# Kernel optimization log

Measured on AMD Instinct MI355X. Metric: run time of the kernel, lower is better.

Reference implementation:

```python
import jax, jax.numpy as jnp
import numpy as np

EPS = 1e-12  # F.normalize eps

def _l2norm(t):
    n = jnp.linalg.norm(t, axis=-1, keepdims=True)
    return t / jnp.maximum(n, EPS)

def setup_inputs() -> dict:
    key = jax.random.key(0)
    ks = jax.random.split(key, 6)
    B, S, H, M = 4, 4096, 1024, 256
    x = jax.random.normal(ks[0], (B, S, H), dtype=jnp.float32)
    W_query = jax.random.normal(ks[1], (M, H), dtype=jnp.float32) * 0.02
    W_key = jax.random.normal(ks[2], (M, H), dtype=jnp.float32) * 0.02
    W_value = jax.random.normal(ks[3], (M, H), dtype=jnp.float32) * 0.02
    W_out = jax.random.normal(ks[4], (H, M), dtype=jnp.float32) * 0.02
    M0 = jnp.zeros((M, M), dtype=jnp.float32)
    return {"x": x, "W_query": W_query, "W_key": W_key, "W_value": W_value,
            "W_out": W_out, "M0": M0, "chunk_size": 64}

def reference(x, W_query, W_key, W_value, W_out, M0, chunk_size):
    B, S, H = x.shape
    Mdim = W_query.shape[0]
    decay, max_m_norm = 0.99, 10.0
    q = jnp.einsum('bsh,mh->bsm', x, W_query)
    k = _l2norm(jnp.einsum('bsh,mh->bsm', x, W_key))
    v = _l2norm(jnp.einsum('bsh,mh->bsm', x, W_value))
    n_chunks = S // chunk_size
    c = chunk_size
    # (n_chunks, B, c, Mdim) so scan iterates over chunks
    qc = q.reshape(B, n_chunks, c, Mdim).transpose(1, 0, 2, 3)
    kc = k.reshape(B, n_chunks, c, Mdim).transpose(1, 0, 2, 3)
    vc = v.reshape(B, n_chunks, c, Mdim).transpose(1, 0, 2, 3)

    def step(Mst, qkv):
        qch, kch, vch = qkv
        # read with state at start of chunk: q @ M.T
        r = jnp.einsum('bcm,nm->bcn', qch, Mst)
        # uniform write, token-level aggregation
        outer = jnp.einsum('bci,bcj->ij', vch, kch) / (B * c)
        Mn = decay * Mst + outer
        nrm = jnp.linalg.norm(Mn)
        Mn = Mn * (max_m_norm / jnp.maximum(nrm, max_m_norm))
        return Mn, r

    _, r_all = jax.lax.scan(step, M0, (qc, kc, vc))  # (n_chunks, B, c, Mdim)
    retrieved = r_all.transpose(1, 0, 2, 3).reshape(B, S, Mdim)
    out = jnp.einsum('bsm,hm->bsh', retrieved, W_out)
    return out
```

## Files before the change

### kernel.cpp

```cpp
#include <hip/hip_runtime.h>


typedef __attribute__((ext_vector_type(4))) float  f4;
typedef __attribute__((ext_vector_type(8))) short  bf16x8;

constexpr int   Hdim  = 1024;
constexpr int   Md    = 256;
constexpr int   Ttok  = 16384;
constexpr float DECAY = 0.99f;
constexpr float MAXN  = 10.0f;

__device__ __forceinline__ unsigned short f2bf(float f) {
  union { float f; unsigned u; } v; v.f = f;
  unsigned r = v.u + 0x7FFFu + ((v.u >> 16) & 1u);
  return (unsigned short)(r >> 16);
}
__device__ __forceinline__ float bf2f(unsigned short h) {
  union { unsigned u; float f; } v; v.u = ((unsigned)h) << 16; return v.f;
}

__global__ __launch_bounds__(256) void k1_proj(
    const float* __restrict__ x, const float* __restrict__ Wq,
    const float* __restrict__ Wk, const float* __restrict__ Wv,
    unsigned short* __restrict__ qp, unsigned short* __restrict__ kb,
    unsigned short* __restrict__ vb)
{
  __shared__ unsigned short Als[128][40];
  __shared__ unsigned short Bls[128][40];
  const int tid  = threadIdx.x;
  const int seg  = blockIdx.x >> 1;
  const int nseg = (blockIdx.x & 1) * 128;
  const int row0 = blockIdx.y * 128;
  const float* Wseg = (seg == 0) ? Wq : ((seg == 1) ? Wk : Wv);
  unsigned short* dst = (seg == 0) ? qp : ((seg == 1) ? kb : vb);

  const int tk = tid & 7, tr = tid >> 3;
  const int lane = tid & 63, wid = tid >> 6;
  const int wm = wid & 1, wn = wid >> 1;
  const int lr = lane & 15, lq = lane >> 4;

  f4 acc[4][4];
#pragma unroll
  for (int i = 0; i < 4; ++i)
#pragma unroll
    for (int j = 0; j < 4; ++j) acc[i][j] = f4{0.f, 0.f, 0.f, 0.f};

  for (int kk = 0; kk < Hdim; kk += 32) {
#pragma unroll
    for (int p = 0; p < 4; ++p) {
      int row = tr + 32 * p;
      float4 av = *(const float4*)&x[(row0 + row) * Hdim + kk + tk * 4];
      ushort4 ua = make_ushort4(f2bf(av.x), f2bf(av.y), f2bf(av.z), f2bf(av.w));
      *(ushort4*)&Als[row][tk * 4] = ua;
      float4 bv = *(const float4*)&Wseg[(nseg + row) * Hdim + kk + tk * 4];
      ushort4 ub = make_ushort4(f2bf(bv.x), f2bf(bv.y), f2bf(bv.z), f2bf(bv.w));
      *(ushort4*)&Bls[row][tk * 4] = ub;
    }
    __syncthreads();
    bf16x8 af[4], bfr[4];
#pragma unroll
    for (int i = 0; i < 4; ++i) af[i]  = *(const bf16x8*)&Als[wm * 64 + i * 16 + lr][lq * 8];
#pragma unroll
    for (int j = 0; j < 4; ++j) bfr[j] = *(const bf16x8*)&Bls[wn * 64 + j * 16 + lr][lq * 8];
#pragma unroll
    for (int i = 0; i < 4; ++i)
#pragma unroll
      for (int j = 0; j < 4; ++j)
        acc[i][j] = __builtin_amdgcn_mfma_f32_16x16x32_bf16(af[i], bfr[j], acc[i][j], 0, 0, 0);
    __syncthreads();
  }
#pragma unroll
  for (int i = 0; i < 4; ++i)
#pragma unroll
    for (int rr = 0; rr < 4; ++rr) {
      int token = row0 + wm * 64 + i * 16 + lq * 4 + rr;
      int b = token >> 12, s = token & 4095;
      int pidx = (s >> 6) * 256 + b * 64 + (s & 63);
#pragma unroll
      for (int j = 0; j < 4; ++j) {
        int n = nseg + wn * 64 + j * 16 + lr;
        dst[pidx * Md + n] = f2bf(acc[i][j][rr]);
      }
    }
}

__global__ __launch_bounds__(256) void k2_norm(unsigned short* __restrict__ kb,
                                               unsigned short* __restrict__ vb)
{
  const int wid = threadIdx.x >> 6, lane = threadIdx.x & 63;
  const int row = blockIdx.x * 4 + wid;
  unsigned short* p = (row < Ttok) ? (kb + row * Md) : (vb + (row - Ttok) * Md);
  ushort4 v = *(ushort4*)&p[lane * 4];
  float f0 = bf2f(v.x), f1 = bf2f(v.y), f2 = bf2f(v.z), f3 = bf2f(v.w);
  float s = f0 * f0 + f1 * f1 + f2 * f2 + f3 * f3;
#pragma unroll
  for (int off = 32; off; off >>= 1) s += __shfl_xor(s, off);
  float inv = 1.0f / fmaxf(sqrtf(s), 1e-12f);
  v = make_ushort4(f2bf(f0 * inv), f2bf(f1 * inv), f2bf(f2 * inv), f2bf(f3 * inv));
  *(ushort4*)&p[lane * 4] = v;
}

__global__ __launch_bounds__(256) void k3_outer(
    const unsigned short* __restrict__ kb, const unsigned short* __restrict__ vb,
    float* __restrict__ O)
{
  __shared__ unsigned short Als[64][40];
  __shared__ unsigned short Bls[256][40];
  const int tid = threadIdx.x;
  const int t  = blockIdx.y;
  const int i0 = blockIdx.x * 64;
  const int lane = tid & 63, wid = tid >> 6;
  const int lr = lane & 15, lq = lane >> 4;

  f4 acc[16];
#pragma unroll
  for (int q = 0; q < 16; ++q) acc[q] = f4{0.f, 0.f, 0.f, 0.f};

  for (int tok0 = 0; tok0 < 256; tok0 += 32) {
    {
      int il = tid & 63, tl0 = tid >> 6;
#pragma unroll
      for (int p = 0; p < 8; ++p) {
        int tl = tl0 + 4 * p;
        Als[il][tl] = vb[(t * 256 + tok0 + tl) * Md + i0 + il];
      }
    }
    {
      int j4 = (tid & 63) * 4, tl0 = tid >> 6;
#pragma unroll
      for (int p = 0; p < 8; ++p) {
        int tl = tl0 + 4 * p;
        ushort4 kv = *(const ushort4*)&kb[(t * 256 + tok0 + tl) * Md + j4];
        Bls[j4 + 0][tl] = kv.x; Bls[j4 + 1][tl] = kv.y;
        Bls[j4 + 2][tl] = kv.z; Bls[j4 + 3][tl] = kv.w;
      }
    }
    __syncthreads();
    bf16x8 af = *(const bf16x8*)&Als[wid * 16 + lr][lq * 8];
#pragma unroll
    for (int j = 0; j < 16; ++j) {
      bf16x8 bfr = *(const bf16x8*)&Bls[j * 16 + lr][lq * 8];
      acc[j] = __builtin_amdgcn_mfma_f32_16x16x32_bf16(af, bfr, acc[j], 0, 0, 0);
    }
    __syncthreads();
  }
  float* Ot = O + t * 65536;
#pragma unroll
  for (int j = 0; j < 16; ++j)
#pragma unroll
    for (int rr = 0; rr < 4; ++rr) {
      int i = i0 + wid * 16 + lq * 4 + rr;
      Ot[i * 256 + j * 16 + lr] = acc[j][rr] * (1.0f / 256.0f);
    }
}

__global__ __launch_bounds__(256) void k4_gram(const float* __restrict__ O, float* __restrict__ D)
{
  __shared__ unsigned short Tls[64][40];
  const int tid = threadIdx.x;
  const int kbase = blockIdx.x * 1024;
  const int lane = tid & 63, wid = tid >> 6;
  const int lr = lane & 15, lq = lane >> 4;
  f4 acc[4];
#pragma unroll
  for (int q = 0; q < 4; ++q) acc[q] = f4{0.f, 0.f, 0.f, 0.f};

  for (int kk = 0; kk < 1024; kk += 32) {
    int tk = tid & 7, tr = tid >> 3;
#pragma unroll
    for (int p = 0; p < 2; ++p) {
      int row = tr + 32 * p;
      float4 v = *(const float4*)&O[(long)row * 65536 + kbase + kk + tk * 4];
      ushort4 u = make_ushort4(f2bf(v.x), f2bf(v.y), f2bf(v.z), f2bf(v.w));
      *(ushort4*)&Tls[row][tk * 4] = u;
    }
    __syncthreads();
    bf16x8 af = *(const bf16x8*)&Tls[wid * 16 + lr][lq * 8];
#pragma unroll
    for (int nt = 0; nt < 4; ++nt) {
      bf16x8 bfr = *(const bf16x8*)&Tls[nt * 16 + lr][lq * 8];
      acc[nt] = __builtin_amdgcn_mfma_f32_16x16x32_bf16(af, bfr, acc[nt], 0, 0, 0);
    }
    __syncthreads();
  }
#pragma unroll
  for (int nt = 0; nt < 4; ++nt)
#pragma unroll
    for (int rr = 0; rr < 4; ++rr)
      atomicAdd(&D[(wid * 16 + lq * 4 + rr) * 64 + nt * 16 + lr], acc[nt][rr]);
}

__global__ __launch_bounds__(64) void k5_scan(const float* __restrict__ D, float* __restrict__ Coef)
{
  __shared__ float Dl[64 * 65];
  const int lane = threadIdx.x;
  for (int it = 0; it < 64; ++it) Dl[it * 65 + lane] = D[it * 64 + lane];
  __syncthreads();
  float c = 0.f, w = 0.f, nm2 = 0.f;
  for (int t = 0; t < 64; ++t) {
    Coef[t * 64 + lane] = c;
    float wt   = __shfl(w, t);
    float Dtt  = Dl[t * 65 + t];
    float nmn2 = DECAY * DECAY * nm2 + 2.f * DECAY * wt + Dtt;
    float nrm  = sqrtf(fmaxf(nmn2, 0.f));
    float s    = MAXN / fmaxf(nrm, MAXN);
    c   = s * (DECAY * c + ((lane == t) ? 1.f : 0.f));
    w   = s * (DECAY * w + Dl[t * 65 + lane]);
    nm2 = s * s * nmn2;
  }
}

__global__ __launch_bounds__(256) void k6_mbuild(const float* __restrict__ O,
    const float* __restrict__ Coef, unsigned short* __restrict__ Mb)
{
  __shared__ float Cl[4096];
  const int tid = threadIdx.x;
  const int col = blockIdx.x * 256 + tid;
  for (int i = tid; i < 4096; i += 256) Cl[i] = Coef[i];
  float ov[64];
#pragma unroll
  for (int j = 0; j < 64; ++j) ov[j] = O[(long)j * 65536 + col];
  __syncthreads();
#pragma unroll
  for (int t = 0; t < 64; ++t) {
    float a = 0.f;
#pragma unroll
    for (int j = 0; j < 64; ++j)
      if (j < t) a += Cl[t * 64 + j] * ov[j];
    Mb[(long)t * 65536 + col] = f2bf(a);
  }
}

__global__ __launch_bounds__(256) void k7_rgemm(
    const unsigned short* __restrict__ qp, const unsigned short* __restrict__ Mb,
    unsigned short* __restrict__ rb)
{
  __shared__ unsigned short Als[128][40];
  __shared__ unsigned short Bls[128][40];
  const int tid = threadIdx.x;
  const int t = blockIdx.z;
  const int row0 = t * 256 + blockIdx.y * 128;
  const int n0 = blockIdx.x * 128;
  const int lane = tid & 63, wid = tid >> 6;
  const int wm = wid & 1, wn = wid >> 1;
  const int lr = lane & 15, lq = lane >> 4;

  f4 acc[4][4];
#pragma unroll
  for (int i = 0; i < 4; ++i)
#pragma unroll
    for (int j = 0; j < 4; ++j) acc[i][j] = f4{0.f, 0.f, 0.f, 0.f};

  for (int kk = 0; kk < 256; kk += 32) {
    int kcol = (tid & 3) * 8, row = tid >> 2;
#pragma unroll
    for (int p = 0; p < 2; ++p) {
      *(bf16x8*)&Als[row + 64 * p][kcol] =
          *(const bf16x8*)&qp[(row0 + row + 64 * p) * Md + kk + kcol];
      *(bf16x8*)&Bls[row + 64 * p][kcol] =
          *(const bf16x8*)&Mb[(long)t * 65536 + (n0 + row + 64 * p) * Md + kk + kcol];
    }
    __syncthreads();
    bf16x8 af[4], bfr[4];
#pragma unroll
    for (int i = 0; i < 4; ++i) af[i]  = *(const bf16x8*)&Als[wm * 64 + i * 16 + lr][lq * 8];
#pragma unroll
    for (int j = 0; j < 4; ++j) bfr[j] = *(const bf16x8*)&Bls[wn * 64 + j * 16 + lr][lq * 8];
#pragma unroll
    for (int i = 0; i < 4; ++i)
#pragma unroll
      for (int j = 0; j < 4; ++j)
        acc[i][j] = __builtin_amdgcn_mfma_f32_16x16x32_bf16(af[i], bfr[j], acc[i][j], 0, 0, 0);
    __syncthreads();
  }
#pragma unroll
  for (int i = 0; i < 4; ++i)
#pragma unroll
    for (int rr = 0; rr < 4; ++rr) {
      int prow = row0 + wm * 64 + i * 16 + lq * 4 + rr;
#pragma unroll
      for (int j = 0; j < 4; ++j) {
        int n = n0 + wn * 64 + j * 16 + lr;
        rb[prow * Md + n] = f2bf(acc[i][j][rr]);
      }
    }
}

__global__ __launch_bounds__(256) void k8_out(
    const unsigned short* __restrict__ rb, const float* __restrict__ Wo,
    float* __restrict__ out)
{
  __shared__ unsigned short Als[128][40];
  __shared__ unsigned short Bls[128][40];
  const int tid = threadIdx.x;
  const int n0 = blockIdx.x * 128;
  const int row0 = blockIdx.y * 128;
  const int lane = tid & 63, wid = tid >> 6;
  const int wm = wid & 1, wn = wid >> 1;
  const int lr = lane & 15, lq = lane >> 4;

  f4 acc[4][4];
#pragma unroll
  for (int i = 0; i < 4; ++i)
#pragma unroll
    for (int j = 0; j < 4; ++j) acc[i][j] = f4{0.f, 0.f, 0.f, 0.f};

  for (int kk = 0; kk < 256; kk += 32) {
    {
      int kcol = (tid & 3) * 8, row = tid >> 2;
#pragma unroll
      for (int p = 0; p < 2; ++p)
        *(bf16x8*)&Als[row + 64 * p][kcol] =
            *(const bf16x8*)&rb[(row0 + row + 64 * p) * Md + kk + kcol];
    }
    {
      int tk = tid & 7, tr = tid >> 3;
#pragma unroll
      for (int p = 0; p < 4; ++p) {
        int row = tr + 32 * p;
        float4 v = *(const float4*)&Wo[(n0 + row) * Md + kk + tk * 4];
        ushort4 u = make_ushort4(f2bf(v.x), f2bf(v.y), f2bf(v.z), f2bf(v.w));
        *(ushort4*)&Bls[row][tk * 4] = u;
      }
    }
    __syncthreads();
    bf16x8 af[4], bfr[4];
#pragma unroll
    for (int i = 0; i < 4; ++i) af[i]  = *(const bf16x8*)&Als[wm * 64 + i * 16 + lr][lq * 8];
#pragma unroll
    for (int j = 0; j < 4; ++j) bfr[j] = *(const bf16x8*)&Bls[wn * 64 + j * 16 + lr][lq * 8];
#pragma unroll
    for (int i = 0; i < 4; ++i)
#pragma unroll
      for (int j = 0; j < 4; ++j)
        acc[i][j] = __builtin_amdgcn_mfma_f32_16x16x32_bf16(af[i], bfr[j], acc[i][j], 0, 0, 0);
    __syncthreads();
  }
#pragma unroll
  for (int i = 0; i < 4; ++i)
#pragma unroll
    for (int rr = 0; rr < 4; ++rr) {
      int pidx = row0 + wm * 64 + i * 16 + lq * 4 + rr;
      int t = pidx >> 8, rm = pidx & 255;
      int token = (rm >> 6) * 4096 + t * 64 + (rm & 63);
#pragma unroll
      for (int j = 0; j < 4; ++j) {
        int h = n0 + wn * 64 + j * 16 + lr;
        out[(long)token * Hdim + h] = acc[i][j][rr];
      }
    }
}

extern "C" void kernel_launch(void* const* d_in, const int* in_sizes, int n_in,
                              void* d_out, int out_size, void* d_ws, size_t ws_size,
                              hipStream_t stream) {
  (void)in_sizes; (void)n_in; (void)out_size; (void)ws_size;
  const float* x  = (const float*)d_in[0];
  const float* Wq = (const float*)d_in[1];
  const float* Wk = (const float*)d_in[2];
  const float* Wv = (const float*)d_in[3];
  const float* Wo = (const float*)d_in[4];
  float* out = (float*)d_out;
  char* ws = (char*)d_ws;

  unsigned short* qp = (unsigned short*)(ws + 0);
  unsigned short* kb = (unsigned short*)(ws + 8388608);
  unsigned short* vb = (unsigned short*)(ws + 16777216);
  float* O    = (float*)(ws + 25165824);
  float* D    = (float*)(ws + 41943040);
  float* Coef = (float*)(ws + 41959424);
  unsigned short* Mb = vb;
  unsigned short* rb = kb;

  hipMemsetAsync(D, 0, 64 * 64 * sizeof(float), stream);
  k1_proj <<<dim3(6, 128),   256, 0, stream>>>(x, Wq, Wk, Wv, qp, kb, vb);
  k2_norm <<<8192,           256, 0, stream>>>(kb, vb);
  k3_outer<<<dim3(4, 64),    256, 0, stream>>>(kb, vb, O);
  k4_gram <<<64,             256, 0, stream>>>(O, D);
  k5_scan <<<1,               64, 0, stream>>>(D, Coef);
  k6_mbuild<<<256,           256, 0, stream>>>(O, Coef, Mb);
  k7_rgemm<<<dim3(2, 2, 64), 256, 0, stream>>>(qp, Mb, rb);
  k8_out  <<<dim3(8, 128),   256, 0, stream>>>(rb, Wo, out);
}
```

Before: 286.8 us.

## Fuse scan into M-build recurrence, defer normalization, XCD-aware tile mapping

Replaces the separate scan and quadratic coefficient build with one kernel. It computes the per-chunk scale factors once and then builds each M state with a linear recurrence instead of a 64x64 coefficient sum. k2 now only computes inverse norms and zeroes D, and k3 applies the scaling while loading tiles, so the extra normalized write-back is gone. It also remaps k1 and k8 blocks so that tiles sharing a row strip land on the same XCD, splits k4 across more blocks, and uses packed bf16 conversion. The cost is some extra multiply and rounding work in k3's loads and more atomics in k4.

```diff
diff --git a/kernel.cpp b/kernel.cpp
--- a/kernel.cpp
+++ b/kernel.cpp
@@ -1,4 +1,5 @@
 #include <hip/hip_runtime.h>
+#include <hip/hip_bf16.h>
 
 
 typedef __attribute__((ext_vector_type(4))) float  f4;
@@ -18,6 +19,10 @@
 __device__ __forceinline__ float bf2f(unsigned short h) {
   union { unsigned u; float f; } v; v.u = ((unsigned)h) << 16; return v.f;
 }
+__device__ __forceinline__ unsigned pk2bf(float a, float b) {
+  __hip_bfloat162 h = __float22bfloat162_rn(make_float2(a, b));
+  unsigned u; __builtin_memcpy(&u, &h, 4); return u;
+}
 
 __global__ __launch_bounds__(256) void k1_proj(
     const float* __restrict__ x, const float* __restrict__ Wq,
@@ -28,9 +33,14 @@
   __shared__ unsigned short Als[128][40];
   __shared__ unsigned short Bls[128][40];
   const int tid  = threadIdx.x;
-  const int seg  = blockIdx.x >> 1;
-  const int nseg = (blockIdx.x & 1) * 128;
-  const int row0 = blockIdx.y * 128;
+  const int g    = blockIdx.x;
+  const int xcd  = g & 7, wq_ = g >> 3;
+  const int ntile = wq_ % 6;
+  const int strip = xcd * 16 + wq_ / 6;
+  const int row0 = strip * 128;
+  const int n0   = ntile * 128;
+  const int seg  = n0 >> 8;
+  const int nw0  = n0 & 255;
   const float* Wseg = (seg == 0) ? Wq : ((seg == 1) ? Wk : Wv);
   unsigned short* dst = (seg == 0) ? qp : ((seg == 1) ? kb : vb);
 
@@ -49,12 +59,10 @@
 #pragma unroll
     for (int p = 0; p < 4; ++p) {
       int row = tr + 32 * p;
-      float4 av = *(const float4*)&x[(row0 + row) * Hdim + kk + tk * 4];
-      ushort4 ua = make_ushort4(f2bf(av.x), f2bf(av.y), f2bf(av.z), f2bf(av.w));
-      *(ushort4*)&Als[row][tk * 4] = ua;
-      float4 bv = *(const float4*)&Wseg[(nseg + row) * Hdim + kk + tk * 4];
-      ushort4 ub = make_ushort4(f2bf(bv.x), f2bf(bv.y), f2bf(bv.z), f2bf(bv.w));
-      *(ushort4*)&Bls[row][tk * 4] = ub;
+      float4 av = *(const float4*)&x[(long)(row0 + row) * Hdim + kk + tk * 4];
+      *(uint2*)&Als[row][tk * 4] = make_uint2(pk2bf(av.x, av.y), pk2bf(av.z, av.w));
+      float4 bv = *(const float4*)&Wseg[(long)(nw0 + row) * Hdim + kk + tk * 4];
+      *(uint2*)&Bls[row][tk * 4] = make_uint2(pk2bf(bv.x, bv.y), pk2bf(bv.z, bv.w));
     }
     __syncthreads();
     bf16x8 af[4], bfr[4];
@@ -78,30 +86,36 @@
       int pidx = (s >> 6) * 256 + b * 64 + (s & 63);
 #pragma unroll
       for (int j = 0; j < 4; ++j) {
-        int n = nseg + wn * 64 + j * 16 + lr;
-        dst[pidx * Md + n] = f2bf(acc[i][j][rr]);
-      }
-    }
-}
-
-__global__ __launch_bounds__(256) void k2_norm(unsigned short* __restrict__ kb,
-                                               unsigned short* __restrict__ vb)
-{
-  const int wid = threadIdx.x >> 6, lane = threadIdx.x & 63;
+        int nn = nw0 + wn * 64 + j * 16 + lr;
+        dst[pidx * Md + nn] = f2bf(acc[i][j][rr]);
+      }
+    }
+}
+
+__global__ __launch_bounds__(256) void k2_norms(
+    const unsigned short* __restrict__ kb, const unsigned short* __restrict__ vb,
+    float* __restrict__ innk, float* __restrict__ innv, float* __restrict__ D)
+{
+  const int tid = threadIdx.x;
+  if (blockIdx.x == 0)
+    for (int i = tid; i < 4096; i += 256) D[i] = 0.f;
+  const int wid = tid >> 6, lane = tid & 63;
   const int row = blockIdx.x * 4 + wid;
-  unsigned short* p = (row < Ttok) ? (kb + row * Md) : (vb + (row - Ttok) * Md);
-  ushort4 v = *(ushort4*)&p[lane * 4];
+  const unsigned short* p = (row < Ttok) ? (kb + (long)row * Md) : (vb + (long)(row - Ttok) * Md);
+  ushort4 v = *(const ushort4*)&p[lane * 4];
   float f0 = bf2f(v.x), f1 = bf2f(v.y), f2 = bf2f(v.z), f3 = bf2f(v.w);
   float s = f0 * f0 + f1 * f1 + f2 * f2 + f3 * f3;
 #pragma unroll
   for (int off = 32; off; off >>= 1) s += __shfl_xor(s, off);
-  float inv = 1.0f / fmaxf(sqrtf(s), 1e-12f);
-  v = make_ushort4(f2bf(f0 * inv), f2bf(f1 * inv), f2bf(f2 * inv), f2bf(f3 * inv));
-  *(ushort4*)&p[lane * 4] = v;
+  if (lane == 0) {
+    float inv = 1.0f / fmaxf(sqrtf(s), 1e-12f);
+    if (row < Ttok) innk[row] = inv; else innv[row - Ttok] = inv;
+  }
 }
 
 __global__ __launch_bounds__(256) void k3_outer(
     const unsigned short* __restrict__ kb, const unsigned short* __restrict__ vb,
+    const float* __restrict__ innk, const float* __restrict__ innv,
     float* __restrict__ O)
 {
   __shared__ unsigned short Als[64][40];
@@ -122,7 +136,9 @@
 #pragma unroll
       for (int p = 0; p < 8; ++p) {
         int tl = tl0 + 4 * p;
-        Als[il][tl] = vb[(t * 256 + tok0 + tl) * Md + i0 + il];
+        int pidx = t * 256 + tok0 + tl;
+        float sc = innv[pidx];
+        Als[il][tl] = f2bf(bf2f(vb[(long)pidx * Md + i0 + il]) * sc);
       }
     }
     {
@@ -130,9 +146,13 @@
 #pragma unroll
       for (int p = 0; p < 8; ++p) {
         int tl = tl0 + 4 * p;
-        ushort4 kv = *(const ushort4*)&kb[(t * 256 + tok0 + tl) * Md + j4];
-        Bls[j4 + 0][tl] = kv.x; Bls[j4 + 1][tl] = kv.y;
-        Bls[j4 + 2][tl] = kv.z; Bls[j4 + 3][tl] = kv.w;
+        int pidx = t * 256 + tok0 + tl;
+        float sc = innk[pidx];
+        ushort4 kv = *(const ushort4*)&kb[(long)pidx * Md + j4];
+        Bls[j4 + 0][tl] = f2bf(bf2f(kv.x) * sc);
+        Bls[j4 + 1][tl] = f2bf(bf2f(kv.y) * sc);
+        Bls[j4 + 2][tl] = f2bf(bf2f(kv.z) * sc);
+        Bls[j4 + 3][tl] = f2bf(bf2f(kv.w) * sc);
       }
     }
     __syncthreads();
@@ -144,7 +164,7 @@
     }
     __syncthreads();
   }
-  float* Ot = O + t * 65536;
+  float* Ot = O + (long)t * 65536;
 #pragma unroll
   for (int j = 0; j < 16; ++j)
 #pragma unroll
@@ -158,21 +178,20 @@
 {
   __shared__ unsigned short Tls[64][40];
   const int tid = threadIdx.x;
-  const int kbase = blockIdx.x * 1024;
+  const int kbase = blockIdx.x * 256;
   const int lane = tid & 63, wid = tid >> 6;
   const int lr = lane & 15, lq = lane >> 4;
   f4 acc[4];
 #pragma unroll
   for (int q = 0; q < 4; ++q) acc[q] = f4{0.f, 0.f, 0.f, 0.f};
 
-  for (int kk = 0; kk < 1024; kk += 32) {
+  for (int kk = 0; kk < 256; kk += 32) {
     int tk = tid & 7, tr = tid >> 3;
 #pragma unroll
     for (int p = 0; p < 2; ++p) {
       int row = tr + 32 * p;
       float4 v = *(const float4*)&O[(long)row * 65536 + kbase + kk + tk * 4];
-      ushort4 u = make_ushort4(f2bf(v.x), f2bf(v.y), f2bf(v.z), f2bf(v.w));
-      *(ushort4*)&Tls[row][tk * 4] = u;
+      *(uint2*)&Tls[row][tk * 4] = make_uint2(pk2bf(v.x, v.y), pk2bf(v.z, v.w));
     }
     __syncthreads();
     bf16x8 af = *(const bf16x8*)&Tls[wid * 16 + lr][lq * 8];
@@ -190,44 +209,38 @@
       atomicAdd(&D[(wid * 16 + lq * 4 + rr) * 64 + nt * 16 + lr], acc[nt][rr]);
 }
 
-__global__ __launch_bounds__(64) void k5_scan(const float* __restrict__ D, float* __restrict__ Coef)
+__global__ __launch_bounds__(256) void k56_mstate(const float* __restrict__ O,
+    const float* __restrict__ D, unsigned short* __restrict__ Mb)
 {
   __shared__ float Dl[64 * 65];
-  const int lane = threadIdx.x;
-  for (int it = 0; it < 64; ++it) Dl[it * 65 + lane] = D[it * 64 + lane];
+  __shared__ float sarr[64];
+  const int tid = threadIdx.x;
+  const int col = blockIdx.x * 256 + tid;
+  float ov[64];
+#pragma unroll
+  for (int j = 0; j < 64; ++j) ov[j] = O[(long)j * 65536 + col];
+  for (int i = tid; i < 4096; i += 256) Dl[(i >> 6) * 65 + (i & 63)] = D[i];
   __syncthreads();
-  float c = 0.f, w = 0.f, nm2 = 0.f;
+  if (tid < 64) {
+    const int lane = tid;
+    float w = 0.f, nm2 = 0.f;
+    for (int t = 0; t < 64; ++t) {
+      float wt   = __shfl(w, t);
+      float Dtt  = Dl[t * 65 + t];
+      float nmn2 = DECAY * DECAY * nm2 + 2.f * DECAY * wt + Dtt;
+      float nrm  = sqrtf(fmaxf(nmn2, 0.f));
+      float s    = MAXN / fmaxf(nrm, MAXN);
+      if (lane == 0) sarr[t] = s;
+      w   = s * (DECAY * w + Dl[t * 65 + lane]);
+      nm2 = s * s * nmn2;
+    }
+  }
+  __syncthreads();
+  float m = 0.f;
+#pragma unroll
   for (int t = 0; t < 64; ++t) {
-    Coef[t * 64 + lane] = c;
-    float wt   = __shfl(w, t);
-    float Dtt  = Dl[t * 65 + t];
-    float nmn2 = DECAY * DECAY * nm2 + 2.f * DECAY * wt + Dtt;
-    float nrm  = sqrtf(fmaxf(nmn2, 0.f));
-    float s    = MAXN / fmaxf(nrm, MAXN);
-    c   = s * (DECAY * c + ((lane == t) ? 1.f : 0.f));
-    w   = s * (DECAY * w + Dl[t * 65 + lane]);
-    nm2 = s * s * nmn2;
-  }
-}
-
-__global__ __launch_bounds__(256) void k6_mbuild(const float* __restrict__ O,
-    const float* __restrict__ Coef, unsigned short* __restrict__ Mb)
-{
-  __shared__ float Cl[4096];
-  const int tid = threadIdx.x;
-  const int col = blockIdx.x * 256 + tid;
-  for (int i = tid; i < 4096; i += 256) Cl[i] = Coef[i];
-  float ov[64];
-#pragma unroll
-  for (int j = 0; j < 64; ++j) ov[j] = O[(long)j * 65536 + col];
-  __syncthreads();
-#pragma unroll
-  for (int t = 0; t < 64; ++t) {
-    float a = 0.f;
-#pragma unroll
-    for (int j = 0; j < 64; ++j)
-      if (j < t) a += Cl[t * 64 + j] * ov[j];
-    Mb[(long)t * 65536 + col] = f2bf(a);
+    Mb[(long)t * 65536 + col] = f2bf(m);
+    m = sarr[t] * (DECAY * m + ov[t]);
   }
 }
 
@@ -256,7 +269,7 @@
 #pragma unroll
     for (int p = 0; p < 2; ++p) {
       *(bf16x8*)&Als[row + 64 * p][kcol] =
-          *(const bf16x8*)&qp[(row0 + row + 64 * p) * Md + kk + kcol];
+          *(const bf16x8*)&qp[(long)(row0 + row + 64 * p) * Md + kk + kcol];
       *(bf16x8*)&Bls[row + 64 * p][kcol] =
           *(const bf16x8*)&Mb[(long)t * 65536 + (n0 + row + 64 * p) * Md + kk + kcol];
     }
@@ -281,7 +294,7 @@
 #pragma unroll
       for (int j = 0; j < 4; ++j) {
         int n = n0 + wn * 64 + j * 16 + lr;
-        rb[prow * Md + n] = f2bf(acc[i][j][rr]);
+        rb[(long)prow * Md + n] = f2bf(acc[i][j][rr]);
       }
     }
 }
@@ -293,8 +306,12 @@
   __shared__ unsigned short Als[128][40];
   __shared__ unsigned short Bls[128][40];
   const int tid = threadIdx.x;
-  const int n0 = blockIdx.x * 128;
-  const int row0 = blockIdx.y * 128;
+  const int g = blockIdx.x;
+  const int xcd = g & 7, wq_ = g >> 3;
+  const int ntile = wq_ & 7;
+  const int strip = xcd * 16 + (wq_ >> 3);
+  const int n0 = ntile * 128;
+  const int row0 = strip * 128;
   const int lane = tid & 63, wid = tid >> 6;
   const int wm = wid & 1, wn = wid >> 1;
   const int lr = lane & 15, lq = lane >> 4;
@@ -311,16 +328,15 @@
 #pragma unroll
       for (int p = 0; p < 2; ++p)
         *(bf16x8*)&Als[row + 64 * p][kcol] =
-            *(const bf16x8*)&rb[(row0 + row + 64 * p) * Md + kk + kcol];
+            *(const bf16x8*)&rb[(long)(row0 + row + 64 * p) * Md + kk + kcol];
     }
     {
       int tk = tid & 7, tr = tid >> 3;
 #pragma unroll
       for (int p = 0; p < 4; ++p) {
         int row = tr + 32 * p;
-        float4 v = *(const float4*)&Wo[(n0 + row) * Md + kk + tk * 4];
-        ushort4 u = make_ushort4(f2bf(v.x), f2bf(v.y), f2bf(v.z), f2bf(v.w));
-        *(ushort4*)&Bls[row][tk * 4] = u;
+        float4 v = *(const float4*)&Wo[(long)(n0 + row) * Md + kk + tk * 4];
+        *(uint2*)&Bls[row][tk * 4] = make_uint2(pk2bf(v.x, v.y), pk2bf(v.z, v.w));
       }
     }
     __syncthreads();
@@ -368,17 +384,16 @@
   unsigned short* vb = (unsigned short*)(ws + 16777216);
   float* O    = (float*)(ws + 25165824);
   float* D    = (float*)(ws + 41943040);
-  float* Coef = (float*)(ws + 41959424);
+  float* innk = (float*)(ws + 41959424);
+  float* innv = (float*)(ws + 42024960);
   unsigned short* Mb = vb;
   unsigned short* rb = kb;
 
-  hipMemsetAsync(D, 0, 64 * 64 * sizeof(float), stream);
-  k1_proj <<<dim3(6, 128),   256, 0, stream>>>(x, Wq, Wk, Wv, qp, kb, vb);
-  k2_norm <<<8192,           256, 0, stream>>>(kb, vb);
-  k3_outer<<<dim3(4, 64),    256, 0, stream>>>(kb, vb, O);
-  k4_gram <<<64,             256, 0, stream>>>(O, D);
-  k5_scan <<<1,               64, 0, stream>>>(D, Coef);
-  k6_mbuild<<<256,           256, 0, stream>>>(O, Coef, Mb);
-  k7_rgemm<<<dim3(2, 2, 64), 256, 0, stream>>>(qp, Mb, rb);
-  k8_out  <<<dim3(8, 128),   256, 0, stream>>>(rb, Wo, out);
-}
+  k1_proj  <<<768,            256, 0, stream>>>(x, Wq, Wk, Wv, qp, kb, vb);
+  k2_norms <<<8192,           256, 0, stream>>>(kb, vb, innk, innv, D);
+  k3_outer <<<dim3(4, 64),    256, 0, stream>>>(kb, vb, innk, innv, O);
+  k4_gram  <<<256,            256, 0, stream>>>(O, D);
+  k56_mstate<<<256,           256, 0, stream>>>(O, D, Mb);
+  k7_rgemm <<<dim3(2, 2, 64), 256, 0, stream>>>(qp, Mb, rb);
+  k8_out   <<<1024,           256, 0, stream>>>(rb, Wo, out);
+}
```

Result: faster. 257.0 us (-10.4%).
